# Kernel optimization log

Hardware: AMD Instinct MI355X
Metric: run time of the kernel (lower is better)

## Reference

```python
import jax, jax.numpy as jnp
import numpy as np

DIM = 1024
N_HEADS = 16
HEAD_DIM = DIM // N_HEADS  # 64
HALF = HEAD_DIM // 2       # 32
DEPTH = 6
N_BRANCH = 2
NEG_INF = -1e9


def _rot_H(x, cos, sin, m):
    # H direction: adjacent-pair complex layout (..., HALF, 2)
    # x: [B,S,H,D], cos/sin: [HALF], m: [B,S] int
    B, S, H, D = x.shape
    xr = x.reshape(B, S, H, HALF, 2)
    re, im = xr[..., 0], xr[..., 1]
    re2 = re * cos - im * sin
    im2 = re * sin + im * cos
    rot = jnp.stack([re2, im2], axis=-1).reshape(B, S, H, D)
    return jnp.where((m != 0)[:, :, None, None], rot, x)


def _rot_B(x, cos, sin, m):
    # B direction: split-half complex layout (real = first half, imag = second half)
    re, im = x[..., :HALF], x[..., HALF:]
    re2 = re * cos - im * sin
    im2 = re * sin + im * cos
    rot = jnp.concatenate([re2, im2], axis=-1)
    return jnp.where((m != 0)[:, :, None, None], rot, x)


def _apply_rope_instructions(x, H_mask, B_mask, freqs_cos, freqs_sin):
    # Sequentially compose rotations per depth level, as in the torch loops.
    for i in range(DEPTH):
        x = _rot_H(x, freqs_cos[1], freqs_sin[1], H_mask[i])
        for b in range(N_BRANCH):
            x = _rot_B(x, freqs_cos[b + 1], freqs_sin[b + 1], B_mask[i, b])
    return x


def setup_inputs() -> dict:
    key = jax.random.key(0)
    ks = jax.random.split(key, 10)
    B, S = 2, 1024
    x = jax.random.normal(ks[0], (B, S, DIM), dtype=jnp.float32)
    masks = jax.random.randint(ks[1], (B, 1, S, S), 0, 2, dtype=jnp.int32)
    H_mask = jax.random.randint(ks[2], (DEPTH, B, S), 0, 2, dtype=jnp.int32)
    B_mask = jax.random.randint(ks[3], (DEPTH, N_BRANCH, B, S), 0, 2, dtype=jnp.int32)
    theta = jax.random.uniform(ks[4], (4, HALF), dtype=jnp.float32) * 2.0 * np.pi
    freqs_cos = jnp.cos(theta)
    freqs_sin = jnp.sin(theta)
    scale = 1.0 / np.sqrt(DIM)
    wq = jax.random.normal(ks[5], (DIM, DIM), dtype=jnp.float32) * scale
    wk = jax.random.normal(ks[6], (DIM, DIM), dtype=jnp.float32) * scale
    wv = jax.random.normal(ks[7], (DIM, DIM), dtype=jnp.float32) * scale
    wo = jax.random.normal(ks[8], (DIM, DIM), dtype=jnp.float32) * scale
    return {"x": x, "masks": masks, "H_mask": H_mask, "B_mask": B_mask,
            "freqs_cos": freqs_cos, "freqs_sin": freqs_sin,
            "wq": wq, "wk": wk, "wv": wv, "wo": wo}


def reference(x, masks, H_mask, B_mask, freqs_cos, freqs_sin, wq, wk, wv, wo):
    B, S, _ = x.shape
    xq = (x @ wq).reshape(B, S, N_HEADS, HEAD_DIM)
    xk = (x @ wk).reshape(B, S, N_HEADS, HEAD_DIM)
    xv = (x @ wv).reshape(B, S, N_HEADS, HEAD_DIM)
    xq = _apply_rope_instructions(xq, H_mask, B_mask, freqs_cos, freqs_sin)
    xk = _apply_rope_instructions(xk, H_mask, B_mask, freqs_cos, freqs_sin)
    scores = jnp.einsum('bqhd,bkhd->bhqk', xq, xk) / np.sqrt(HEAD_DIM)
    scores = jnp.where(masks == 0, NEG_INF, scores)
    probs = jax.nn.softmax(scores, axis=-1)
    out = jnp.einsum('bhqk,bkhd->bqhd', probs, xv).reshape(B, S, DIM)
    return out @ wo
```

## Files before the change

kernel.cpp:

```cpp
#include <hip/hip_runtime.h>

#define SLEN 1024
#define BATCH 2
#define DEPTH 6

typedef _Float16 h8 __attribute__((ext_vector_type(8)));
typedef float    f4 __attribute__((ext_vector_type(4)));
#define MF16(a, b, c) __builtin_amdgcn_mfma_f32_16x16x32_f16(a, b, c, 0, 0, 0)

#define SW(row, c) (((c) ^ ((row) & 7)) * 8)

__device__ __forceinline__ void async_cp16(const _Float16* g, _Float16* l) {
  __builtin_amdgcn_global_load_lds(
      (const __attribute__((address_space(1))) void*)g,
      (__attribute__((address_space(3))) void*)l, 16, 0, 0);
}

__global__ __launch_bounds__(256) void prep(const float* __restrict__ x,
    const float* __restrict__ wq, const float* __restrict__ wk,
    const float* __restrict__ wv, const float* __restrict__ wo,
    const int* __restrict__ masks, _Float16* __restrict__ xh,
    _Float16* __restrict__ qt, _Float16* __restrict__ kt,
    _Float16* __restrict__ vt, _Float16* __restrict__ ot,
    unsigned int* __restrict__ mpk) {
  __shared__ _Float16 T[64][72];
  const int bid = blockIdx.x, t = threadIdx.x;
  if (bid < 1024) {
    int idx = (bid * 256 + t) * 8;
    float4 f0 = *(const float4*)(x + idx);
    float4 f1 = *(const float4*)(x + idx + 4);
    union { h8 v; _Float16 e[8]; } u;
    u.e[0] = (_Float16)f0.x; u.e[1] = (_Float16)f0.y;
    u.e[2] = (_Float16)f0.z; u.e[3] = (_Float16)f0.w;
    u.e[4] = (_Float16)f1.x; u.e[5] = (_Float16)f1.y;
    u.e[6] = (_Float16)f1.z; u.e[7] = (_Float16)f1.w;
    *(h8*)(xh + idx) = u.v;
  } else if (bid < 2048) {
    const int i = bid - 1024;
    const int wsel = i >> 8;
    const float* W = wsel == 0 ? wq : wsel == 1 ? wk : wsel == 2 ? wv : wo;
    _Float16* O = wsel == 0 ? qt : wsel == 1 ? kt : wsel == 2 ? vt : ot;
    const int k0 = ((i >> 4) & 15) * 64, n0 = (i & 15) * 64;
    const int rr = t >> 2, cs = (t & 3) * 16;
    #pragma unroll
    for (int j = 0; j < 4; ++j) {
      float4 f = *(const float4*)(W + (size_t)(k0 + rr) * 1024 + n0 + cs + j * 4);
      T[rr][cs + j * 4 + 0] = (_Float16)f.x;
      T[rr][cs + j * 4 + 1] = (_Float16)f.y;
      T[rr][cs + j * 4 + 2] = (_Float16)f.z;
      T[rr][cs + j * 4 + 3] = (_Float16)f.w;
    }
    __syncthreads();
    const int n = t >> 2, ks = (t & 3) * 16;
    union { h8 v; _Float16 e[8]; } u0, u1;
    #pragma unroll
    for (int j = 0; j < 8; ++j) { u0.e[j] = T[ks + j][n]; u1.e[j] = T[ks + 8 + j][n]; }
    *(h8*)(O + (size_t)(n0 + n) * 1024 + k0 + ks)     = u0.v;
    *(h8*)(O + (size_t)(n0 + n) * 1024 + k0 + ks + 8) = u1.v;
  } else {
    const int g = (bid - 2048) * 256 + t;
    const int row = g >> 5, w = g & 31;
    const int* m = masks + (size_t)row * 1024 + w * 32;
    unsigned int bits = 0;
    #pragma unroll
    for (int j4 = 0; j4 < 8; ++j4) {
      int4 mm = *(const int4*)(m + j4 * 4);
      if (mm.x) bits |= 1u << (j4 * 4 + 0);
      if (mm.y) bits |= 1u << (j4 * 4 + 1);
      if (mm.z) bits |= 1u << (j4 * 4 + 2);
      if (mm.w) bits |= 1u << (j4 * 4 + 3);
    }
    mpk[g] = bits;
  }
}

template <int TMODE, typename CT>
__device__ __forceinline__ void gemm16(const _Float16* __restrict__ A,
                                       const _Float16* __restrict__ Bt,
                                       CT* __restrict__ C) {
  __shared__ _Float16 As[128 * 64];
  __shared__ _Float16 Bs[128 * 64];
  const int t    = threadIdx.x;
  const int bm   = blockIdx.y * 128, bn = blockIdx.x * 128;
  const int w    = t >> 6, lane = t & 63;
  const int ln15 = lane & 15, quad = lane >> 4;
  const int wm   = (w >> 1) * 64, wn = (w & 1) * 64;
  const int srow8 = lane >> 3;
  const int sch   = (lane & 7) ^ srow8;
  const _Float16* agp = A  + (size_t)(bm + w * 32 + srow8) * 1024 + sch * 8;
  const _Float16* bgp = Bt + (size_t)(bn + w * 32 + srow8) * 1024 + sch * 8;
  _Float16* alds = As + w * 2048;
  _Float16* blds = Bs + w * 2048;

  f4 acc[4][4];
  #pragma unroll
  for (int i = 0; i < 4; ++i)
    #pragma unroll
    for (int j = 0; j < 4; ++j) acc[i][j] = (f4){0.f, 0.f, 0.f, 0.f};

  for (int k0 = 0; k0 < 1024; k0 += 64) {
    #pragma unroll
    for (int j = 0; j < 4; ++j) {
      async_cp16(agp + k0 + j * 8192, alds + j * 512);
      async_cp16(bgp + k0 + j * 8192, blds + j * 512);
    }
    __syncthreads();
    #pragma unroll
    for (int kk8 = 0; kk8 < 8; kk8 += 4) {
      h8 af[4], bf[4];
      #pragma unroll
      for (int i = 0; i < 4; ++i) {
        int row = wm + i * 16 + ln15;
        af[i] = *(const h8*)&As[row * 64 + SW(row, kk8 + quad)];
      }
      #pragma unroll
      for (int j = 0; j < 4; ++j) {
        int row = wn + j * 16 + ln15;
        bf[j] = *(const h8*)&Bs[row * 64 + SW(row, kk8 + quad)];
      }
      #pragma unroll
      for (int i = 0; i < 4; ++i)
        #pragma unroll
        for (int j = 0; j < 4; ++j)
          acc[i][j] = MF16(af[i], bf[j], acc[i][j]);
    }
    __syncthreads();
  }
  if (TMODE == 0) {
    #pragma unroll
    for (int i = 0; i < 4; ++i) {
      int row = bm + wm + i * 16 + quad * 4;
      #pragma unroll
      for (int r = 0; r < 4; ++r)
        #pragma unroll
        for (int j = 0; j < 4; ++j)
          C[(size_t)(row + r) * 1024 + bn + wn + j * 16 + ln15] = (CT)acc[i][j][r];
    }
  } else {
    #pragma unroll
    for (int i = 0; i < 4; ++i) {
      int m0 = bm + wm + i * 16 + quad * 4;
      #pragma unroll
      for (int r = 0; r < 4; ++r) {
        int m = m0 + r;
        size_t base = ((size_t)(m >> 10) * 1024) * 1024 + (m & 1023);
        #pragma unroll
        for (int j = 0; j < 4; ++j)
          C[base + (size_t)(bn + wn + j * 16 + ln15) * 1024] = (CT)acc[i][j][r];
      }
    }
  }
}

__global__ __launch_bounds__(256) void gemm_qkv16(const _Float16* __restrict__ xh,
    const _Float16* __restrict__ qt, const _Float16* __restrict__ kt,
    const _Float16* __restrict__ vtw, _Float16* __restrict__ q,
    _Float16* __restrict__ k, _Float16* __restrict__ vth) {
  if (blockIdx.z == 2)      gemm16<1, _Float16>(xh, vtw, vth);
  else if (blockIdx.z == 1) gemm16<0, _Float16>(xh, kt, k);
  else                      gemm16<0, _Float16>(xh, qt, q);
}

__global__ __launch_bounds__(256) void gemm_o16(const _Float16* __restrict__ A,
    const _Float16* __restrict__ Bt, float* __restrict__ C) {
  gemm16<0, float>(A, Bt, C);
}

__global__ __launch_bounds__(256) void rope_kernel(_Float16* __restrict__ qf,
    _Float16* __restrict__ kf, const int* __restrict__ Hm,
    const int* __restrict__ Bm, const float* __restrict__ fc,
    const float* __restrict__ fs) {
  __shared__ float c1[32], s1[32], c2[32], s2[32];
  const int t = threadIdx.x;
  if (t < 32) {
    c1[t] = fc[32 + t]; s1[t] = fs[32 + t];
    c2[t] = fc[64 + t]; s2[t] = fs[64 + t];
  }
  __syncthreads();
  const int gid = blockIdx.x * 256 + t;
  const int bs  = gid >> 4;
  _Float16* base = (blockIdx.y == 0 ? qf : kf) + (size_t)gid * 64;
  float vv[64];
  #pragma unroll
  for (int i = 0; i < 8; ++i) {
    union { h8 v; _Float16 e[8]; } u;
    u.v = *(const h8*)(base + i * 8);
    #pragma unroll
    for (int j = 0; j < 8; ++j) vv[i * 8 + j] = (float)u.e[j];
  }
  #pragma unroll 1
  for (int d = 0; d < DEPTH; ++d) {
    if (Hm[d * (BATCH * SLEN) + bs] != 0) {
      #pragma unroll
      for (int j = 0; j < 32; ++j) {
        float re = vv[2 * j], im = vv[2 * j + 1];
        vv[2 * j]     = re * c1[j] - im * s1[j];
        vv[2 * j + 1] = re * s1[j] + im * c1[j];
      }
    }
    if (Bm[(d * 2 + 0) * (BATCH * SLEN) + bs] != 0) {
      #pragma unroll
      for (int j = 0; j < 32; ++j) {
        float re = vv[j], im = vv[j + 32];
        vv[j]      = re * c1[j] - im * s1[j];
        vv[j + 32] = re * s1[j] + im * c1[j];
      }
    }
    if (Bm[(d * 2 + 1) * (BATCH * SLEN) + bs] != 0) {
      #pragma unroll
      for (int j = 0; j < 32; ++j) {
        float re = vv[j], im = vv[j + 32];
        vv[j]      = re * c2[j] - im * s2[j];
        vv[j + 32] = re * s2[j] + im * c2[j];
      }
    }
  }
  #pragma unroll
  for (int i = 0; i < 8; ++i) {
    union { h8 v; _Float16 e[8]; } u;
    #pragma unroll
    for (int j = 0; j < 8; ++j) u.e[j] = (_Float16)vv[i * 8 + j];
    *(h8*)(base + i * 8) = u.v;
  }
}

__global__ __launch_bounds__(256) void attn_mfma(const _Float16* __restrict__ qh,
    const _Float16* __restrict__ kh, const _Float16* __restrict__ vth,
    const unsigned int* __restrict__ mpk, _Float16* __restrict__ out) {
  __shared__ _Float16 Ks[64 * 64];
  __shared__ _Float16 Vs[64 * 64];
  __shared__ _Float16 QP[4][16][72];

  const int t    = threadIdx.x;
  const int w    = t >> 6, lane = t & 63;
  const int ln15 = lane & 15, quad = lane >> 4;

  const int bh = blockIdx.x & 31;
  const int s0 = (blockIdx.x >> 5) * 64;
  const int b = bh >> 4, h = bh & 15;
  const size_t qkbase = (size_t)b * (SLEN * 1024) + h * 64;
  const size_t vbase  = ((size_t)b * 1024 + h * 64) * SLEN;

  {
    const int srow = t >> 2, sc0 = (t & 3) * 16;
    const _Float16* src = qh + qkbase + (size_t)(s0 + srow) * 1024 + sc0;
    *(h8*)&QP[w][srow & 15][sc0]     = *(const h8*)src;
    *(h8*)&QP[w][srow & 15][sc0 + 8] = *(const h8*)(src + 8);
  }
  h8 aq0 = *(h8*)&QP[w][ln15][quad * 8];
  h8 aq1 = *(h8*)&QP[w][ln15][32 + quad * 8];

  const int srow8 = lane >> 3;
  const int sch   = (lane & 7) ^ srow8;
  const _Float16* kgp = kh + qkbase + (size_t)(w * 16 + srow8) * 1024 + sch * 8;
  const _Float16* vgp = vth + vbase + (size_t)(w * 16 + srow8) * 1024 + sch * 8;
  _Float16* klds = Ks + w * 1024;
  _Float16* vlds = Vs + w * 1024;

  const unsigned int* mp = mpk + ((size_t)b * SLEN + s0 + w * 16 + quad * 4) * 32;

  float lrow[4] = {1e-30f, 1e-30f, 1e-30f, 1e-30f};
  f4 oacc[4];
  #pragma unroll
  for (int f = 0; f < 4; ++f) oacc[f] = (f4){0.f, 0.f, 0.f, 0.f};

  for (int c = 0; c < 16; ++c) {
    const int kc = c * 64;
    async_cp16(kgp + (size_t)kc * 1024,        klds);
    async_cp16(kgp + (size_t)kc * 1024 + 8192, klds + 512);
    async_cp16(vgp + kc,                       vlds);
    async_cp16(vgp + kc + 8192,                vlds + 512);
    unsigned int w0[4], w1[4];
    #pragma unroll
    for (int r = 0; r < 4; ++r) {
      w0[r] = mp[r * 32 + c * 2];
      w1[r] = mp[r * 32 + c * 2 + 1];
    }
    __syncthreads();

    f4 s[4];
    #pragma unroll
    for (int f = 0; f < 4; ++f) {
      int row = f * 16 + ln15;
      h8 bk0 = *(const h8*)&Ks[row * 64 + SW(row, quad)];
      h8 bk1 = *(const h8*)&Ks[row * 64 + SW(row, 4 + quad)];
      f4 acc = (f4){0.f, 0.f, 0.f, 0.f};
      acc = MF16(aq0, bk0, acc);
      acc = MF16(aq1, bk1, acc);
      s[f] = acc;
    }
    #pragma unroll
    for (int f = 0; f < 4; ++f) {
      const int col = f * 16 + ln15;
      #pragma unroll
      for (int r = 0; r < 4; ++r) {
        unsigned int wd = (col & 32) ? w1[r] : w0[r];
        float p = ((wd >> (col & 31)) & 1u)
                    ? __expf(s[f][r] * 0.125f - 3.0f) : 0.0f;
        lrow[r] += p;
        QP[w][quad * 4 + r][col] = (_Float16)p;
      }
    }
    h8 ap0 = *(h8*)&QP[w][ln15][quad * 8];
    h8 ap1 = *(h8*)&QP[w][ln15][32 + quad * 8];
    #pragma unroll
    for (int f = 0; f < 4; ++f) {
      int row = f * 16 + ln15;
      h8 bv0 = *(const h8*)&Vs[row * 64 + SW(row, quad)];
      h8 bv1 = *(const h8*)&Vs[row * 64 + SW(row, 4 + quad)];
      f4 o = oacc[f];
      o = MF16(ap0, bv0, o);
      o = MF16(ap1, bv1, o);
      oacc[f] = o;
    }
    __syncthreads();
  }

  #pragma unroll
  for (int r = 0; r < 4; ++r) {
    float sm = lrow[r];
    sm += __shfl_xor(sm, 1);
    sm += __shfl_xor(sm, 2);
    sm += __shfl_xor(sm, 4);
    sm += __shfl_xor(sm, 8);
    lrow[r] = 1.0f / sm;
  }
  #pragma unroll
  for (int f = 0; f < 4; ++f)
    #pragma unroll
    for (int r = 0; r < 4; ++r)
      QP[w][quad * 4 + r][f * 16 + ln15] = (_Float16)(oacc[f][r] * lrow[r]);
  const int orow = lane >> 2, oseg = (lane & 3) * 16;
  _Float16* op = out + qkbase + (size_t)(s0 + w * 16 + orow) * 1024 + oseg;
  *(h8*)op       = *(h8*)&QP[w][orow][oseg];
  *(h8*)(op + 8) = *(h8*)&QP[w][orow][oseg + 8];
}

extern "C" void kernel_launch(void* const* d_in, const int* in_sizes, int n_in,
                              void* d_out, int out_size, void* d_ws, size_t ws_size,
                              hipStream_t stream) {
  const float* x     = (const float*)d_in[0];
  const int*   masks = (const int*)d_in[1];
  const int*   Hm    = (const int*)d_in[2];
  const int*   Bm    = (const int*)d_in[3];
  const float* fc    = (const float*)d_in[4];
  const float* fs    = (const float*)d_in[5];
  const float* wq    = (const float*)d_in[6];
  const float* wk    = (const float*)d_in[7];
  const float* wv    = (const float*)d_in[8];
  const float* wo    = (const float*)d_in[9];
  float* out = (float*)d_out;

  _Float16* xh   = (_Float16*)d_ws;
  _Float16* wqt  = xh + (1 << 21);
  _Float16* wkt  = wqt + (1 << 20);
  _Float16* wvt  = wkt + (1 << 20);
  _Float16* wot  = wvt + (1 << 20);
  _Float16* qhh  = wot + (1 << 20);
  _Float16* khh  = qhh + (1 << 21);
  _Float16* vth  = khh + (1 << 21);
  _Float16* aoh  = vth + (1 << 21);
  unsigned int* mpk = (unsigned int*)(aoh + (1 << 21));

  dim3 blk(256);
  prep<<<dim3(2304), blk, 0, stream>>>(x, wq, wk, wv, wo, masks,
                                       xh, wqt, wkt, wvt, wot, mpk);
  gemm_qkv16<<<dim3(8, 16, 3), blk, 0, stream>>>(xh, wqt, wkt, wvt, qhh, khh, vth);
  rope_kernel<<<dim3(128, 2), blk, 0, stream>>>(qhh, khh, Hm, Bm, fc, fs);
  attn_mfma<<<dim3(512), blk, 0, stream>>>(qhh, khh, vth, mpk, aoh);
  gemm_o16<<<dim3(8, 16), blk, 0, stream>>>(aoh, wot, out);
}
```

Before: 172.2 us.

## Fuse RoPE into QK projection epilogue and double-buffer K/V tiles in attention

The separate rope kernel is removed. The Q and K GEMM blocks now stage their fp16 tile in shared memory, and each thread applies the depth-composed rotations to one head row before writing it out. This saves a launch and a full read/write pass over Q and K, at the cost of a longer GEMM epilogue and a possible drop in occupancy. The attention kernel also double-buffers the K/V shared-memory tiles and mask words, so it prefetches the next chunk while computing the current one. That doubles K/V LDS usage and keeps one barrier per iteration.

```diff
diff --git a/kernel.cpp b/kernel.cpp
--- a/kernel.cpp
+++ b/kernel.cpp
@@ -77,14 +77,27 @@
 template <int TMODE, typename CT>
 __device__ __forceinline__ void gemm16(const _Float16* __restrict__ A,
                                        const _Float16* __restrict__ Bt,
-                                       CT* __restrict__ C) {
-  __shared__ _Float16 As[128 * 64];
-  __shared__ _Float16 Bs[128 * 64];
+                                       CT* __restrict__ C,
+                                       const int* __restrict__ Hm,
+                                       const int* __restrict__ Bm,
+                                       const float* __restrict__ fc,
+                                       const float* __restrict__ fs) {
+  __shared__ _Float16 SH[16384];
+  __shared__ float FR[128];
+  _Float16* As = SH;
+  _Float16* Bs = SH + 8192;
   const int t    = threadIdx.x;
   const int bm   = blockIdx.y * 128, bn = blockIdx.x * 128;
   const int w    = t >> 6, lane = t & 63;
   const int ln15 = lane & 15, quad = lane >> 4;
   const int wm   = (w >> 1) * 64, wn = (w & 1) * 64;
+
+  if (TMODE == 2 && t < 128) {
+    int g = t & 31;
+    FR[t] = (t < 32) ? fc[32 + g] : (t < 64) ? fs[32 + g]
+          : (t < 96) ? fc[64 + g] : fs[64 + g];
+  }
+
   const int srow8 = lane >> 3;
   const int sch   = (lane & 7) ^ srow8;
   const _Float16* agp = A  + (size_t)(bm + w * 32 + srow8) * 1024 + sch * 8;
@@ -126,6 +139,7 @@
     }
     __syncthreads();
   }
+
   if (TMODE == 0) {
     #pragma unroll
     for (int i = 0; i < 4; ++i) {
@@ -136,7 +150,7 @@
         for (int j = 0; j < 4; ++j)
           C[(size_t)(row + r) * 1024 + bn + wn + j * 16 + ln15] = (CT)acc[i][j][r];
     }
-  } else {
+  } else if (TMODE == 1) {
     #pragma unroll
     for (int i = 0; i < 4; ++i) {
       int m0 = bm + wm + i * 16 + quad * 4;
@@ -149,86 +163,93 @@
           C[base + (size_t)(bn + wn + j * 16 + ln15) * 1024] = (CT)acc[i][j][r];
       }
     }
+  } else {
+    #pragma unroll
+    for (int i = 0; i < 4; ++i)
+      #pragma unroll
+      for (int j = 0; j < 4; ++j) {
+        int cl = wn + j * 16 + ln15;
+        #pragma unroll
+        for (int r = 0; r < 4; ++r) {
+          int rl = wm + i * 16 + quad * 4 + r;
+          SH[rl * 128 + (((cl >> 3) ^ (rl & 15)) << 3) + (cl & 7)] =
+              (_Float16)acc[i][j][r];
+        }
+      }
+    __syncthreads();
+    const int row = t >> 1, head = t & 1;
+    const int bs = bm + row;
+    float vv[64];
+    #pragma unroll
+    for (int cc = 0; cc < 8; ++cc) {
+      int phys = (head * 8 + cc) ^ (row & 15);
+      union { h8 v; _Float16 e[8]; } u;
+      u.v = *(const h8*)&SH[row * 128 + phys * 8];
+      #pragma unroll
+      for (int e = 0; e < 8; ++e) vv[cc * 8 + e] = (float)u.e[e];
+    }
+    #pragma unroll 1
+    for (int d = 0; d < DEPTH; ++d) {
+      if (Hm[d * (BATCH * SLEN) + bs] != 0) {
+        #pragma unroll
+        for (int j = 0; j < 32; ++j) {
+          float re = vv[2 * j], im = vv[2 * j + 1];
+          vv[2 * j]     = re * FR[j] - im * FR[32 + j];
+          vv[2 * j + 1] = re * FR[32 + j] + im * FR[j];
+        }
+      }
+      if (Bm[(d * 2 + 0) * (BATCH * SLEN) + bs] != 0) {
+        #pragma unroll
+        for (int j = 0; j < 32; ++j) {
+          float re = vv[j], im = vv[j + 32];
+          vv[j]      = re * FR[j] - im * FR[32 + j];
+          vv[j + 32] = re * FR[32 + j] + im * FR[j];
+        }
+      }
+      if (Bm[(d * 2 + 1) * (BATCH * SLEN) + bs] != 0) {
+        #pragma unroll
+        for (int j = 0; j < 32; ++j) {
+          float re = vv[j], im = vv[j + 32];
+          vv[j]      = re * FR[64 + j] - im * FR[96 + j];
+          vv[j + 32] = re * FR[96 + j] + im * FR[64 + j];
+        }
+      }
+    }
+    _Float16* dst = (_Float16*)C + (size_t)(bm + row) * 1024 + bn + head * 64;
+    #pragma unroll
+    for (int cc = 0; cc < 8; ++cc) {
+      union { h8 v; _Float16 e[8]; } u;
+      #pragma unroll
+      for (int e = 0; e < 8; ++e) u.e[e] = (_Float16)vv[cc * 8 + e];
+      *(h8*)(dst + cc * 8) = u.v;
+    }
   }
 }
 
 __global__ __launch_bounds__(256) void gemm_qkv16(const _Float16* __restrict__ xh,
     const _Float16* __restrict__ qt, const _Float16* __restrict__ kt,
     const _Float16* __restrict__ vtw, _Float16* __restrict__ q,
-    _Float16* __restrict__ k, _Float16* __restrict__ vth) {
-  if (blockIdx.z == 2)      gemm16<1, _Float16>(xh, vtw, vth);
-  else if (blockIdx.z == 1) gemm16<0, _Float16>(xh, kt, k);
-  else                      gemm16<0, _Float16>(xh, qt, q);
+    _Float16* __restrict__ k, _Float16* __restrict__ vth,
+    const int* __restrict__ Hm, const int* __restrict__ Bm,
+    const float* __restrict__ fc, const float* __restrict__ fs) {
+  if (blockIdx.z == 2)
+    gemm16<1, _Float16>(xh, vtw, vth, nullptr, nullptr, nullptr, nullptr);
+  else if (blockIdx.z == 1)
+    gemm16<2, _Float16>(xh, kt, k, Hm, Bm, fc, fs);
+  else
+    gemm16<2, _Float16>(xh, qt, q, Hm, Bm, fc, fs);
 }
 
 __global__ __launch_bounds__(256) void gemm_o16(const _Float16* __restrict__ A,
     const _Float16* __restrict__ Bt, float* __restrict__ C) {
-  gemm16<0, float>(A, Bt, C);
-}
-
-__global__ __launch_bounds__(256) void rope_kernel(_Float16* __restrict__ qf,
-    _Float16* __restrict__ kf, const int* __restrict__ Hm,
-    const int* __restrict__ Bm, const float* __restrict__ fc,
-    const float* __restrict__ fs) {
-  __shared__ float c1[32], s1[32], c2[32], s2[32];
-  const int t = threadIdx.x;
-  if (t < 32) {
-    c1[t] = fc[32 + t]; s1[t] = fs[32 + t];
-    c2[t] = fc[64 + t]; s2[t] = fs[64 + t];
-  }
-  __syncthreads();
-  const int gid = blockIdx.x * 256 + t;
-  const int bs  = gid >> 4;
-  _Float16* base = (blockIdx.y == 0 ? qf : kf) + (size_t)gid * 64;
-  float vv[64];
-  #pragma unroll
-  for (int i = 0; i < 8; ++i) {
-    union { h8 v; _Float16 e[8]; } u;
-    u.v = *(const h8*)(base + i * 8);
-    #pragma unroll
-    for (int j = 0; j < 8; ++j) vv[i * 8 + j] = (float)u.e[j];
-  }
-  #pragma unroll 1
-  for (int d = 0; d < DEPTH; ++d) {
-    if (Hm[d * (BATCH * SLEN) + bs] != 0) {
-      #pragma unroll
-      for (int j = 0; j < 32; ++j) {
-        float re = vv[2 * j], im = vv[2 * j + 1];
-        vv[2 * j]     = re * c1[j] - im * s1[j];
-        vv[2 * j + 1] = re * s1[j] + im * c1[j];
-      }
-    }
-    if (Bm[(d * 2 + 0) * (BATCH * SLEN) + bs] != 0) {
-      #pragma unroll
-      for (int j = 0; j < 32; ++j) {
-        float re = vv[j], im = vv[j + 32];
-        vv[j]      = re * c1[j] - im * s1[j];
-        vv[j + 32] = re * s1[j] + im * c1[j];
-      }
-    }
-    if (Bm[(d * 2 + 1) * (BATCH * SLEN) + bs] != 0) {
-      #pragma unroll
-      for (int j = 0; j < 32; ++j) {
-        float re = vv[j], im = vv[j + 32];
-        vv[j]      = re * c2[j] - im * s2[j];
-        vv[j + 32] = re * s2[j] + im * c2[j];
-      }
-    }
-  }
-  #pragma unroll
-  for (int i = 0; i < 8; ++i) {
-    union { h8 v; _Float16 e[8]; } u;
-    #pragma unroll
-    for (int j = 0; j < 8; ++j) u.e[j] = (_Float16)vv[i * 8 + j];
-    *(h8*)(base + i * 8) = u.v;
-  }
+  gemm16<0, float>(A, Bt, C, nullptr, nullptr, nullptr, nullptr);
 }
 
 __global__ __launch_bounds__(256) void attn_mfma(const _Float16* __restrict__ qh,
     const _Float16* __restrict__ kh, const _Float16* __restrict__ vth,
     const unsigned int* __restrict__ mpk, _Float16* __restrict__ out) {
-  __shared__ _Float16 Ks[64 * 64];
-  __shared__ _Float16 Vs[64 * 64];
+  __shared__ _Float16 Ks[2][64 * 64];
+  __shared__ _Float16 Vs[2][64 * 64];
   __shared__ _Float16 QP[4][16][72];
 
   const int t    = threadIdx.x;
@@ -254,8 +275,6 @@
   const int sch   = (lane & 7) ^ srow8;
   const _Float16* kgp = kh + qkbase + (size_t)(w * 16 + srow8) * 1024 + sch * 8;
   const _Float16* vgp = vth + vbase + (size_t)(w * 16 + srow8) * 1024 + sch * 8;
-  _Float16* klds = Ks + w * 1024;
-  _Float16* vlds = Vs + w * 1024;
 
   const unsigned int* mp = mpk + ((size_t)b * SLEN + s0 + w * 16 + quad * 4) * 32;
 
@@ -264,26 +283,38 @@
   #pragma unroll
   for (int f = 0; f < 4; ++f) oacc[f] = (f4){0.f, 0.f, 0.f, 0.f};
 
+  async_cp16(kgp,        &Ks[0][w * 1024]);
+  async_cp16(kgp + 8192, &Ks[0][w * 1024 + 512]);
+  async_cp16(vgp,        &Vs[0][w * 1024]);
+  async_cp16(vgp + 8192, &Vs[0][w * 1024 + 512]);
+  unsigned int w0[4], w1[4];
+  #pragma unroll
+  for (int r = 0; r < 4; ++r) { w0[r] = mp[r * 32]; w1[r] = mp[r * 32 + 1]; }
+  __syncthreads();
+
   for (int c = 0; c < 16; ++c) {
-    const int kc = c * 64;
-    async_cp16(kgp + (size_t)kc * 1024,        klds);
-    async_cp16(kgp + (size_t)kc * 1024 + 8192, klds + 512);
-    async_cp16(vgp + kc,                       vlds);
-    async_cp16(vgp + kc + 8192,                vlds + 512);
-    unsigned int w0[4], w1[4];
-    #pragma unroll
-    for (int r = 0; r < 4; ++r) {
-      w0[r] = mp[r * 32 + c * 2];
-      w1[r] = mp[r * 32 + c * 2 + 1];
-    }
-    __syncthreads();
+    const int cur = c & 1;
+    unsigned int nw0[4], nw1[4];
+    if (c < 15) {
+      const size_t ko = (size_t)((c + 1) * 64) * 1024;
+      const int    vo = (c + 1) * 64;
+      async_cp16(kgp + ko,        &Ks[cur ^ 1][w * 1024]);
+      async_cp16(kgp + ko + 8192, &Ks[cur ^ 1][w * 1024 + 512]);
+      async_cp16(vgp + vo,        &Vs[cur ^ 1][w * 1024]);
+      async_cp16(vgp + vo + 8192, &Vs[cur ^ 1][w * 1024 + 512]);
+      #pragma unroll
+      for (int r = 0; r < 4; ++r) {
+        nw0[r] = mp[r * 32 + (c + 1) * 2];
+        nw1[r] = mp[r * 32 + (c + 1) * 2 + 1];
+      }
+    }
 
     f4 s[4];
     #pragma unroll
     for (int f = 0; f < 4; ++f) {
       int row = f * 16 + ln15;
-      h8 bk0 = *(const h8*)&Ks[row * 64 + SW(row, quad)];
-      h8 bk1 = *(const h8*)&Ks[row * 64 + SW(row, 4 + quad)];
+      h8 bk0 = *(const h8*)&Ks[cur][row * 64 + SW(row, quad)];
+      h8 bk1 = *(const h8*)&Ks[cur][row * 64 + SW(row, 4 + quad)];
       f4 acc = (f4){0.f, 0.f, 0.f, 0.f};
       acc = MF16(aq0, bk0, acc);
       acc = MF16(aq1, bk1, acc);
@@ -306,12 +337,16 @@
     #pragma unroll
     for (int f = 0; f < 4; ++f) {
       int row = f * 16 + ln15;
-      h8 bv0 = *(const h8*)&Vs[row * 64 + SW(row, quad)];
-      h8 bv1 = *(const h8*)&Vs[row * 64 + SW(row, 4 + quad)];
+      h8 bv0 = *(const h8*)&Vs[cur][row * 64 + SW(row, quad)];
+      h8 bv1 = *(const h8*)&Vs[cur][row * 64 + SW(row, 4 + quad)];
       f4 o = oacc[f];
       o = MF16(ap0, bv0, o);
       o = MF16(ap1, bv1, o);
       oacc[f] = o;
+    }
+    if (c < 15) {
+      #pragma unroll
+      for (int r = 0; r < 4; ++r) { w0[r] = nw0[r]; w1[r] = nw1[r]; }
     }
     __syncthreads();
   }
@@ -365,8 +400,8 @@
   dim3 blk(256);
   prep<<<dim3(2304), blk, 0, stream>>>(x, wq, wk, wv, wo, masks,
                                        xh, wqt, wkt, wvt, wot, mpk);
-  gemm_qkv16<<<dim3(8, 16, 3), blk, 0, stream>>>(xh, wqt, wkt, wvt, qhh, khh, vth);
-  rope_kernel<<<dim3(128, 2), blk, 0, stream>>>(qhh, khh, Hm, Bm, fc, fs);
+  gemm_qkv16<<<dim3(8, 16, 3), blk, 0, stream>>>(xh, wqt, wkt, wvt, qhh, khh,
+                                                 vth, Hm, Bm, fc, fs);
   attn_mfma<<<dim3(512), blk, 0, stream>>>(qhh, khh, vth, mpk, aoh);
   gemm_o16<<<dim3(8, 16), blk, 0, stream>>>(aoh, wot, out);
 }
```

New measurement: 184.5 us. 7.1% more time.

## Double-buffer K/V tiles in attention and halve GEMM M-tile for more blocks

Applied to the files above, without the earlier changes.

The attention kernel gets ping-pong LDS buffers for the K and V tiles and the mask words, so the next chunk is prefetched while the current one is computed. This is meant to hide global-load latency behind the MFMA work. The GEMMs switch from 128x128 to 64x128 tiles and the grid doubles in M, giving more blocks to fill the CUs on small matrices. The cost is lower per-block reuse and a larger LDS footprint in attention. The attention loop keeps only one barrier per iteration while the async prefetch is in flight, which relies on the hardware's waitcnt ordering at that barrier.

```diff
diff --git a/kernel.cpp b/kernel.cpp
--- a/kernel.cpp
+++ b/kernel.cpp
@@ -8,7 +8,7 @@
 typedef float    f4 __attribute__((ext_vector_type(4)));
 #define MF16(a, b, c) __builtin_amdgcn_mfma_f32_16x16x32_f16(a, b, c, 0, 0, 0)
 
-#define SW(row, c) (((c) ^ ((row) & 7)) * 8)
+#define SW(row, c) ((((c) ^ ((row) & 7))) * 8)
 
 __device__ __forceinline__ void async_cp16(const _Float16* g, _Float16* l) {
   __builtin_amdgcn_global_load_lds(
@@ -77,58 +77,60 @@
 template <int TMODE, typename CT>
 __device__ __forceinline__ void gemm16(const _Float16* __restrict__ A,
                                        const _Float16* __restrict__ Bt,
-                                       CT* __restrict__ C) {
-  __shared__ _Float16 As[128 * 64];
-  __shared__ _Float16 Bs[128 * 64];
+                                       CT* __restrict__ C,
+                                       _Float16* __restrict__ SH) {
+  _Float16* As = SH;
+  _Float16* Bs = SH + 4096;
   const int t    = threadIdx.x;
-  const int bm   = blockIdx.y * 128, bn = blockIdx.x * 128;
+  const int bm   = blockIdx.y * 64, bn = blockIdx.x * 128;
   const int w    = t >> 6, lane = t & 63;
   const int ln15 = lane & 15, quad = lane >> 4;
-  const int wm   = (w >> 1) * 64, wn = (w & 1) * 64;
+  const int wm   = (w >> 1) * 32, wn = (w & 1) * 64;
+
   const int srow8 = lane >> 3;
   const int sch   = (lane & 7) ^ srow8;
-  const _Float16* agp = A  + (size_t)(bm + w * 32 + srow8) * 1024 + sch * 8;
+  const _Float16* agp = A  + (size_t)(bm + w * 16 + srow8) * 1024 + sch * 8;
   const _Float16* bgp = Bt + (size_t)(bn + w * 32 + srow8) * 1024 + sch * 8;
-  _Float16* alds = As + w * 2048;
-  _Float16* blds = Bs + w * 2048;
-
-  f4 acc[4][4];
-  #pragma unroll
-  for (int i = 0; i < 4; ++i)
+
+  f4 acc[2][4];
+  #pragma unroll
+  for (int i = 0; i < 2; ++i)
     #pragma unroll
     for (int j = 0; j < 4; ++j) acc[i][j] = (f4){0.f, 0.f, 0.f, 0.f};
 
   for (int k0 = 0; k0 < 1024; k0 += 64) {
     #pragma unroll
-    for (int j = 0; j < 4; ++j) {
-      async_cp16(agp + k0 + j * 8192, alds + j * 512);
-      async_cp16(bgp + k0 + j * 8192, blds + j * 512);
-    }
+    for (int j = 0; j < 2; ++j)
+      async_cp16(agp + k0 + j * 8192, As + w * 1024 + j * 512);
+    #pragma unroll
+    for (int j = 0; j < 4; ++j)
+      async_cp16(bgp + k0 + j * 8192, Bs + w * 2048 + j * 512);
     __syncthreads();
     #pragma unroll
-    for (int kk8 = 0; kk8 < 8; kk8 += 4) {
-      h8 af[4], bf[4];
-      #pragma unroll
-      for (int i = 0; i < 4; ++i) {
+    for (int kk = 0; kk < 8; kk += 4) {
+      h8 af[2], bf[4];
+      #pragma unroll
+      for (int i = 0; i < 2; ++i) {
         int row = wm + i * 16 + ln15;
-        af[i] = *(const h8*)&As[row * 64 + SW(row, kk8 + quad)];
+        af[i] = *(const h8*)&As[row * 64 + SW(row, kk + quad)];
       }
       #pragma unroll
       for (int j = 0; j < 4; ++j) {
         int row = wn + j * 16 + ln15;
-        bf[j] = *(const h8*)&Bs[row * 64 + SW(row, kk8 + quad)];
-      }
-      #pragma unroll
-      for (int i = 0; i < 4; ++i)
+        bf[j] = *(const h8*)&Bs[row * 64 + SW(row, kk + quad)];
+      }
+      #pragma unroll
+      for (int i = 0; i < 2; ++i)
         #pragma unroll
         for (int j = 0; j < 4; ++j)
           acc[i][j] = MF16(af[i], bf[j], acc[i][j]);
     }
     __syncthreads();
   }
+
   if (TMODE == 0) {
     #pragma unroll
-    for (int i = 0; i < 4; ++i) {
+    for (int i = 0; i < 2; ++i) {
       int row = bm + wm + i * 16 + quad * 4;
       #pragma unroll
       for (int r = 0; r < 4; ++r)
@@ -138,7 +140,7 @@
     }
   } else {
     #pragma unroll
-    for (int i = 0; i < 4; ++i) {
+    for (int i = 0; i < 2; ++i) {
       int m0 = bm + wm + i * 16 + quad * 4;
       #pragma unroll
       for (int r = 0; r < 4; ++r) {
@@ -152,18 +154,22 @@
   }
 }
 
-__global__ __launch_bounds__(256) void gemm_qkv16(const _Float16* __restrict__ xh,
-    const _Float16* __restrict__ qt, const _Float16* __restrict__ kt,
-    const _Float16* __restrict__ vtw, _Float16* __restrict__ q,
-    _Float16* __restrict__ k, _Float16* __restrict__ vth) {
-  if (blockIdx.z == 2)      gemm16<1, _Float16>(xh, vtw, vth);
-  else if (blockIdx.z == 1) gemm16<0, _Float16>(xh, kt, k);
-  else                      gemm16<0, _Float16>(xh, qt, q);
-}
-
-__global__ __launch_bounds__(256) void gemm_o16(const _Float16* __restrict__ A,
-    const _Float16* __restrict__ Bt, float* __restrict__ C) {
-  gemm16<0, float>(A, Bt, C);
+__global__ __launch_bounds__(256) void gemm_qkv16(
+    const _Float16* __restrict__ xh, const _Float16* __restrict__ qt,
+    const _Float16* __restrict__ kt, const _Float16* __restrict__ vtw,
+    _Float16* __restrict__ q, _Float16* __restrict__ k,
+    _Float16* __restrict__ vth) {
+  __shared__ _Float16 SH[12288];
+  if (blockIdx.z == 2)      gemm16<1, _Float16>(xh, vtw, vth, SH);
+  else if (blockIdx.z == 1) gemm16<0, _Float16>(xh, kt, k, SH);
+  else                      gemm16<0, _Float16>(xh, qt, q, SH);
+}
+
+__global__ __launch_bounds__(256) void gemm_o16(
+    const _Float16* __restrict__ A, const _Float16* __restrict__ Bt,
+    float* __restrict__ C) {
+  __shared__ _Float16 SH[12288];
+  gemm16<0, float>(A, Bt, C, SH);
 }
 
 __global__ __launch_bounds__(256) void rope_kernel(_Float16* __restrict__ qf,
@@ -227,8 +233,8 @@
 __global__ __launch_bounds__(256) void attn_mfma(const _Float16* __restrict__ qh,
     const _Float16* __restrict__ kh, const _Float16* __restrict__ vth,
     const unsigned int* __restrict__ mpk, _Float16* __restrict__ out) {
-  __shared__ _Float16 Ks[64 * 64];
-  __shared__ _Float16 Vs[64 * 64];
+  __shared__ _Float16 Ks[2][64 * 64];
+  __shared__ _Float16 Vs[2][64 * 64];
   __shared__ _Float16 QP[4][16][72];
 
   const int t    = threadIdx.x;
@@ -254,8 +260,6 @@
   const int sch   = (lane & 7) ^ srow8;
   const _Float16* kgp = kh + qkbase + (size_t)(w * 16 + srow8) * 1024 + sch * 8;
   const _Float16* vgp = vth + vbase + (size_t)(w * 16 + srow8) * 1024 + sch * 8;
-  _Float16* klds = Ks + w * 1024;
-  _Float16* vlds = Vs + w * 1024;
 
   const unsigned int* mp = mpk + ((size_t)b * SLEN + s0 + w * 16 + quad * 4) * 32;
 
@@ -264,26 +268,38 @@
   #pragma unroll
   for (int f = 0; f < 4; ++f) oacc[f] = (f4){0.f, 0.f, 0.f, 0.f};
 
+  async_cp16(kgp,        &Ks[0][w * 1024]);
+  async_cp16(kgp + 8192, &Ks[0][w * 1024 + 512]);
+  async_cp16(vgp,        &Vs[0][w * 1024]);
+  async_cp16(vgp + 8192, &Vs[0][w * 1024 + 512]);
+  unsigned int w0[4], w1[4];
+  #pragma unroll
+  for (int r = 0; r < 4; ++r) { w0[r] = mp[r * 32]; w1[r] = mp[r * 32 + 1]; }
+  __syncthreads();
+
   for (int c = 0; c < 16; ++c) {
-    const int kc = c * 64;
-    async_cp16(kgp + (size_t)kc * 1024,        klds);
-    async_cp16(kgp + (size_t)kc * 1024 + 8192, klds + 512);
-    async_cp16(vgp + kc,                       vlds);
-    async_cp16(vgp + kc + 8192,                vlds + 512);
-    unsigned int w0[4], w1[4];
-    #pragma unroll
-    for (int r = 0; r < 4; ++r) {
-      w0[r] = mp[r * 32 + c * 2];
-      w1[r] = mp[r * 32 + c * 2 + 1];
-    }
-    __syncthreads();
+    const int cur = c & 1;
+    unsigned int nw0[4], nw1[4];
+    if (c < 15) {
+      const size_t ko = (size_t)((c + 1) * 64) * 1024;
+      const int    vo = (c + 1) * 64;
+      async_cp16(kgp + ko,        &Ks[cur ^ 1][w * 1024]);
+      async_cp16(kgp + ko + 8192, &Ks[cur ^ 1][w * 1024 + 512]);
+      async_cp16(vgp + vo,        &Vs[cur ^ 1][w * 1024]);
+      async_cp16(vgp + vo + 8192, &Vs[cur ^ 1][w * 1024 + 512]);
+      #pragma unroll
+      for (int r = 0; r < 4; ++r) {
+        nw0[r] = mp[r * 32 + (c + 1) * 2];
+        nw1[r] = mp[r * 32 + (c + 1) * 2 + 1];
+      }
+    }
 
     f4 s[4];
     #pragma unroll
     for (int f = 0; f < 4; ++f) {
       int row = f * 16 + ln15;
-      h8 bk0 = *(const h8*)&Ks[row * 64 + SW(row, quad)];
-      h8 bk1 = *(const h8*)&Ks[row * 64 + SW(row, 4 + quad)];
+      h8 bk0 = *(const h8*)&Ks[cur][row * 64 + SW(row, quad)];
+      h8 bk1 = *(const h8*)&Ks[cur][row * 64 + SW(row, 4 + quad)];
       f4 acc = (f4){0.f, 0.f, 0.f, 0.f};
       acc = MF16(aq0, bk0, acc);
       acc = MF16(aq1, bk1, acc);
@@ -306,12 +322,16 @@
     #pragma unroll
     for (int f = 0; f < 4; ++f) {
       int row = f * 16 + ln15;
-      h8 bv0 = *(const h8*)&Vs[row * 64 + SW(row, quad)];
-      h8 bv1 = *(const h8*)&Vs[row * 64 + SW(row, 4 + quad)];
+      h8 bv0 = *(const h8*)&Vs[cur][row * 64 + SW(row, quad)];
+      h8 bv1 = *(const h8*)&Vs[cur][row * 64 + SW(row, 4 + quad)];
       f4 o = oacc[f];
       o = MF16(ap0, bv0, o);
       o = MF16(ap1, bv1, o);
       oacc[f] = o;
+    }
+    if (c < 15) {
+      #pragma unroll
+      for (int r = 0; r < 4; ++r) { w0[r] = nw0[r]; w1[r] = nw1[r]; }
     }
     __syncthreads();
   }
@@ -365,8 +385,9 @@
   dim3 blk(256);
   prep<<<dim3(2304), blk, 0, stream>>>(x, wq, wk, wv, wo, masks,
                                        xh, wqt, wkt, wvt, wot, mpk);
-  gemm_qkv16<<<dim3(8, 16, 3), blk, 0, stream>>>(xh, wqt, wkt, wvt, qhh, khh, vth);
+  gemm_qkv16<<<dim3(8, 32, 3), blk, 0, stream>>>(xh, wqt, wkt, wvt,
+                                                 qhh, khh, vth);
   rope_kernel<<<dim3(128, 2), blk, 0, stream>>>(qhh, khh, Hm, Bm, fc, fs);
   attn_mfma<<<dim3(512), blk, 0, stream>>>(qhh, khh, vth, mpk, aoh);
-  gemm_o16<<<dim3(8, 16), blk, 0, stream>>>(aoh, wot, out);
-}
+  gemm_o16<<<dim3(8, 32), blk, 0, stream>>>(aoh, wot, out);
+}
```

Measured after the change: 166.5 us. 3.3% less time.
